# Performance work log

Measured on AMD Instinct MI355X. Metric: run time of the kernel, lower is better.

The kernel has to match this reference:

```python
import jax, jax.numpy as jnp
import numpy as np
from jax import lax

DUNITS = 1024
ATT_DIM = 512
EPROJS = 512
ACONV_CHANS = 10
ACONV_FILTS = 100  # kernel size = 2*100+1 = 201
H_LEN = 16384
N_PREV = 128
SCALING = 2.0


def setup_inputs() -> dict:
    key = jax.random.key(0)
    ks = jax.random.split(key, 10)
    inv = lambda fan_in: 1.0 / np.sqrt(fan_in)
    return {
        "dec_z": jax.random.normal(ks[0], (1, DUNITS), jnp.float32),
        "att_prev": jax.random.uniform(ks[1], (N_PREV, 1, H_LEN), jnp.float32) / H_LEN,
        "pre_compute_enc_h": jax.random.normal(ks[2], (1, H_LEN, ATT_DIM), jnp.float32),
        "enc_h": jax.random.normal(ks[3], (1, H_LEN, EPROJS), jnp.float32),
        "mask": jnp.zeros((1, H_LEN), jnp.float32),
        # parameters (torch default inits, scale by 1/sqrt(fan_in))
        "loc_conv_w": jax.random.normal(ks[4], (ACONV_CHANS, 1, 2 * ACONV_FILTS + 1), jnp.float32) * inv(2 * ACONV_FILTS + 1),
        "mlp_att_w": jax.random.normal(ks[5], (ATT_DIM, ACONV_CHANS), jnp.float32) * inv(ACONV_CHANS),
        "mlp_dec_w": jax.random.normal(ks[6], (ATT_DIM, DUNITS), jnp.float32) * inv(DUNITS),
        "gvec_w": jax.random.normal(ks[7], (1, ATT_DIM), jnp.float32) * inv(ATT_DIM),
        "gvec_b": jnp.zeros((1,), jnp.float32),
    }


def reference(dec_z, att_prev, pre_compute_enc_h, enc_h, mask,
              loc_conv_w, mlp_att_w, mlp_dec_w, gvec_w, gvec_b):
    h_length = enc_h.shape[1]
    dec_z = dec_z.reshape(1, DUNITS)

    # coverage vector: sum of all previous attention distributions -> [1, h]
    cov_vec = jnp.sum(att_prev, axis=0)

    # location conv: Conv2d(1, C, (1, 2F+1)) on [1,1,1,h] == 1D conv on [1,1,h]
    att_conv = lax.conv_general_dilated(
        cov_vec[:, None, :], loc_conv_w,
        window_strides=(1,), padding=[(ACONV_FILTS, ACONV_FILTS)],
        dimension_numbers=("NCH", "OIH", "NCH"),
    )  # [1, C, h]
    # squeeze/transpose then mlp_att (no bias): [1, h, att_dim]
    att_conv = jnp.einsum("bch,ac->bha", att_conv, mlp_att_w)

    # mlp_dec (no bias), tiled over h: [1, 1, att_dim]
    dec_z_tiled = (dec_z @ mlp_dec_w.T)[:, None, :]

    # additive attention score e: [1, h]
    t = jnp.tanh(att_conv + pre_compute_enc_h + dec_z_tiled)
    e = jnp.einsum("bha,oa->bho", t, gvec_w)[..., 0] + gvec_b
    e = e + mask

    w = jax.nn.softmax(SCALING * e, axis=1)  # [1, h]

    att_prev_new = jnp.concatenate([att_prev, w[None]], axis=0)  # [n+1, 1, h]
    c = jnp.sum(enc_h * w[:, :, None], axis=1)  # [1, eprojs]
    return (c, att_prev_new)
```

## Files before the change

### kernel.cpp

```cpp
#include <hip/hip_runtime.h>

#define H_LEN 16384
#define ATT_DIM 512
#define DUNITS 1024
#define EPROJS 512
#define NCH 10
#define KFILT 201
#define PAD 100
#define N_PREV 128
#define NB_SCORE 512
#define NB_CTX 256

__global__ __launch_bounds__(256) void k_prep(const float* __restrict__ att_prev,
                                              const float* __restrict__ mlp_dec_w,
                                              const float* __restrict__ dec_z,
                                              float* __restrict__ out_prev,
                                              float* __restrict__ cov4,
                                              float* __restrict__ dz,
                                              float* __restrict__ out_c) {
    int b = blockIdx.x, tid = threadIdx.x;
    if (b < 256) {
        int h = (b >> 2) * 256 + tid;
        int n0 = (b & 3) * 32;
        float s = 0.f;
        #pragma unroll
        for (int n = n0; n < n0 + 32; ++n) {
            float v = att_prev[n * H_LEN + h];
            s += v;
            out_prev[n * H_LEN + h] = v;
        }
        cov4[(b & 3) * H_LEN + h] = s;
    } else if (b < 384) {
        int lane = tid & 63;
        int a = (b - 256) * 4 + (tid >> 6);
        const float* row = mlp_dec_w + a * DUNITS;
        float s = 0.f;
        #pragma unroll
        for (int t = 0; t < DUNITS / 64; ++t) s += row[lane + 64 * t] * dec_z[lane + 64 * t];
        #pragma unroll
        for (int off = 32; off > 0; off >>= 1) s += __shfl_xor(s, off, 64);
        if (lane == 0) dz[a] = s;
    } else {
        out_c[tid] = 0.f;
        out_c[tid + 256] = 0.f;
    }
}

__global__ __launch_bounds__(256, 2) void k_score(const float* __restrict__ cov4,
                                                  const float* __restrict__ cw,
                                                  const float* __restrict__ pre,
                                                  const float* __restrict__ mask,
                                                  const float* __restrict__ dz,
                                                  const float* __restrict__ watt,
                                                  const float* __restrict__ gv,
                                                  const float* __restrict__ gb,
                                                  float* __restrict__ vbuf,
                                                  float* __restrict__ pm,
                                                  float* __restrict__ ps) {
    __shared__ float cov_s[32 + 2 * PAD];
    __shared__ float mask_s[32];
    __shared__ float pc[4][NCH][32];
    __shared__ float cf[NCH][32];
    __shared__ float vt[32];

    int tid = threadIdx.x, b = blockIdx.x;
    int h0 = b * 32;
    int lane = tid & 63, wv = tid >> 6;
    int a0 = lane * 4;

    for (int i = tid; i < 32 + 2 * PAD; i += 256) {
        int g = h0 - PAD + i;
        float s = 0.f;
        if (g >= 0 && g < H_LEN)
            s = cov4[g] + cov4[H_LEN + g] + cov4[2 * H_LEN + g] + cov4[3 * H_LEN + g];
        cov_s[i] = s;
    }
    if (tid < 32) mask_s[tid] = mask[h0 + tid];

    const float4* pre4 = (const float4*)pre;
    int hbase = h0 + wv * 8;
    float4 P[16];
    #pragma unroll
    for (int j = 0; j < 8; ++j) {
        P[2 * j]     = pre4[(hbase + j) * 128 + lane];
        P[2 * j + 1] = pre4[(hbase + j) * 128 + 64 + lane];
    }

    float Wr[8][NCH], dzr[8], gvr[8];
    #pragma unroll
    for (int i = 0; i < 8; ++i) {
        int a = (i < 4) ? (a0 + i) : (a0 + 256 + (i - 4));
        dzr[i] = dz[a];
        gvr[i] = gv[a];
        #pragma unroll
        for (int c = 0; c < NCH; ++c) Wr[i][c] = watt[a * NCH + c];
    }
    float bias = gb[0];
    __syncthreads();

    {
        int h = tid & 31, q = tid >> 5;
        int k0 = (q * KFILT) / 8, k1 = ((q + 1) * KFILT) / 8;
        float acc[NCH];
        #pragma unroll
        for (int c = 0; c < NCH; ++c) acc[c] = 0.f;
        for (int k = k0; k < k1; ++k) {
            float s = cov_s[h + k];
            #pragma unroll
            for (int c = 0; c < NCH; ++c) acc[c] += s * cw[c * KFILT + k];
        }
        #pragma unroll
        for (int c = 0; c < NCH; ++c) pc[q & 3][c][h] = acc[c];
        __syncthreads();
        if (q >= 4) {
            #pragma unroll
            for (int c = 0; c < NCH; ++c) atomicAdd(&pc[q & 3][c][h], 0.f);
        }
    }
    __syncthreads();
    for (int i = tid; i < NCH * 32; i += 256) {
        int c = i >> 5, h = i & 31;
        cf[c][h] = pc[0][c][h] + pc[1][c][h] + pc[2][c][h] + pc[3][c][h];
    }
    __syncthreads();

    #pragma unroll
    for (int j = 0; j < 8; ++j) {
        int hh = wv * 8 + j;
        float ch[NCH];
        #pragma unroll
        for (int c = 0; c < NCH; ++c) ch[c] = cf[c][hh];
        float4 c0 = P[2 * j], c1 = P[2 * j + 1];
        float pv[8] = {c0.x, c0.y, c0.z, c0.w, c1.x, c1.y, c1.z, c1.w};
        float eacc = 0.f;
        #pragma unroll
        for (int i = 0; i < 8; ++i) {
            float x = pv[i] + dzr[i];
            #pragma unroll
            for (int c = 0; c < NCH; ++c) x += ch[c] * Wr[i][c];
            x = fminf(fmaxf(x, -15.f), 15.f);
            float z = __expf(2.f * x);
            float t = (z - 1.f) * __builtin_amdgcn_rcpf(z + 1.f);
            eacc += t * gvr[i];
        }
        #pragma unroll
        for (int off = 32; off > 0; off >>= 1) eacc += __shfl_xor(eacc, off, 64);
        if (lane == 0) {
            float v = 2.f * (eacc + bias + mask_s[hh]);
            vt[hh] = v;
            vbuf[h0 + hh] = v;
        }
    }
    __syncthreads();

    if (wv == 0) {
        float v = (lane < 32) ? vt[lane] : -1e30f;
        float m = v;
        #pragma unroll
        for (int off = 32; off > 0; off >>= 1) m = fmaxf(m, __shfl_xor(m, off, 64));
        float s = (lane < 32) ? __expf(v - m) : 0.f;
        #pragma unroll
        for (int off = 32; off > 0; off >>= 1) s += __shfl_xor(s, off, 64);
        if (lane == 0) { pm[b] = m; ps[b] = s; }
    }
}

__global__ __launch_bounds__(512) void k_ctx(const float* __restrict__ vbuf,
                                             const float* __restrict__ pm,
                                             const float* __restrict__ ps,
                                             const float* __restrict__ enc,
                                             float* __restrict__ out_w,
                                             float* __restrict__ out_c) {
    __shared__ float redA[8], redB[8];
    __shared__ float wlds[64];
    int tid = threadIdx.x, b = blockIdx.x;
    int lane = tid & 63, wv = tid >> 6;
    int h0 = b * 64;

    float pmv = pm[tid], psv = ps[tid];
    float m = pmv;
    #pragma unroll
    for (int off = 32; off > 0; off >>= 1) m = fmaxf(m, __shfl_xor(m, off, 64));
    if (lane == 0) redA[wv] = m;
    __syncthreads();
    float M = redA[0];
    #pragma unroll
    for (int i = 1; i < 8; ++i) M = fmaxf(M, redA[i]);
    float s = psv * __expf(pmv - M);
    #pragma unroll
    for (int off = 32; off > 0; off >>= 1) s += __shfl_xor(s, off, 64);
    if (lane == 0) redB[wv] = s;
    __syncthreads();
    float S = 0.f;
    #pragma unroll
    for (int i = 0; i < 8; ++i) S += redB[i];
    float rinv = 1.f / S;

    if (tid < 64) {
        float w = __expf(vbuf[h0 + tid] - M) * rinv;
        out_w[h0 + tid] = w;
        wlds[tid] = w;
    }
    __syncthreads();
    float acc = 0.f;
    #pragma unroll 8
    for (int i = 0; i < 64; ++i) acc += wlds[i] * enc[(h0 + i) * EPROJS + tid];
    atomicAdd(&out_c[tid], acc);
}

extern "C" void kernel_launch(void* const* d_in, const int* in_sizes, int n_in,
                              void* d_out, int out_size, void* d_ws, size_t ws_size,
                              hipStream_t stream) {
    const float* dec_z      = (const float*)d_in[0];
    const float* att_prev   = (const float*)d_in[1];
    const float* pre        = (const float*)d_in[2];
    const float* enc_h      = (const float*)d_in[3];
    const float* mask       = (const float*)d_in[4];
    const float* loc_conv_w = (const float*)d_in[5];
    const float* mlp_att_w  = (const float*)d_in[6];
    const float* mlp_dec_w  = (const float*)d_in[7];
    const float* gvec_w     = (const float*)d_in[8];
    const float* gvec_b     = (const float*)d_in[9];

    float* out_c    = (float*)d_out;
    float* out_prev = out_c + EPROJS;
    float* out_w    = out_prev + N_PREV * H_LEN;

    float* ws   = (float*)d_ws;
    float* cov4 = ws;
    float* dz   = cov4 + 4 * H_LEN;
    float* vb   = dz + ATT_DIM;
    float* pm   = vb + H_LEN;
    float* ps   = pm + NB_SCORE;

    k_prep<<<385, 256, 0, stream>>>(att_prev, mlp_dec_w, dec_z, out_prev, cov4, dz, out_c);
    k_score<<<NB_SCORE, 256, 0, stream>>>(cov4, loc_conv_w, pre, mask, dz, mlp_att_w,
                                          gvec_w, gvec_b, vb, pm, ps);
    k_ctx<<<NB_CTX, 512, 0, stream>>>(vb, pm, ps, enc_h, out_w, out_c);
}
```

Baseline: 145.9 us.

## Fuse context accumulation into score kernel using flash-style partial softmax rescaling

Each score block now multiplies its local unnormalized exp weights against its 32 rows of enc_h and writes a per-block partial context vector. A small final kernel computes the global max and sum, rescales each block's partial, and atomically accumulates into the output. This moves the enc_h read into the score kernel, where it can overlap with the tanh work, and shrinks the last kernel to a reduction. The conv partial-sum step also drops the LDS atomic trick in favour of an 8-way buffer. The cost is an extra 1 MB workspace for the partials and more register pressure in k_score.

```diff
diff --git a/kernel.cpp b/kernel.cpp
--- a/kernel.cpp
+++ b/kernel.cpp
@@ -9,7 +9,7 @@
 #define PAD 100
 #define N_PREV 128
 #define NB_SCORE 512
-#define NB_CTX 256
+#define NB_FIN 256
 
 __global__ __launch_bounds__(256) void k_prep(const float* __restrict__ att_prev,
                                               const float* __restrict__ mlp_dec_w,
@@ -54,14 +54,17 @@
                                                   const float* __restrict__ watt,
                                                   const float* __restrict__ gv,
                                                   const float* __restrict__ gb,
+                                                  const float* __restrict__ enc,
                                                   float* __restrict__ vbuf,
                                                   float* __restrict__ pm,
-                                                  float* __restrict__ ps) {
+                                                  float* __restrict__ ps,
+                                                  float* __restrict__ pcb) {
     __shared__ float cov_s[32 + 2 * PAD];
     __shared__ float mask_s[32];
-    __shared__ float pc[4][NCH][32];
+    __shared__ float pc[8][NCH][32];
     __shared__ float cf[NCH][32];
     __shared__ float vt[32];
+    __shared__ float wt[32];
 
     int tid = threadIdx.x, b = blockIdx.x;
     int h0 = b * 32;
@@ -110,17 +113,15 @@
             for (int c = 0; c < NCH; ++c) acc[c] += s * cw[c * KFILT + k];
         }
         #pragma unroll
-        for (int c = 0; c < NCH; ++c) pc[q & 3][c][h] = acc[c];
-        __syncthreads();
-        if (q >= 4) {
-            #pragma unroll
-            for (int c = 0; c < NCH; ++c) atomicAdd(&pc[q & 3][c][h], 0.f);
-        }
+        for (int c = 0; c < NCH; ++c) pc[q][c][h] = acc[c];
     }
     __syncthreads();
     for (int i = tid; i < NCH * 32; i += 256) {
         int c = i >> 5, h = i & 31;
-        cf[c][h] = pc[0][c][h] + pc[1][c][h] + pc[2][c][h] + pc[3][c][h];
+        float s = 0.f;
+        #pragma unroll
+        for (int q = 0; q < 8; ++q) s += pc[q][c][h];
+        cf[c][h] = s;
     }
     __syncthreads();
 
@@ -158,54 +159,65 @@
         float m = v;
         #pragma unroll
         for (int off = 32; off > 0; off >>= 1) m = fmaxf(m, __shfl_xor(m, off, 64));
-        float s = (lane < 32) ? __expf(v - m) : 0.f;
+        float ev = (lane < 32) ? __expf(v - m) : 0.f;
+        if (lane < 32) wt[lane] = ev;
+        float s = ev;
         #pragma unroll
         for (int off = 32; off > 0; off >>= 1) s += __shfl_xor(s, off, 64);
         if (lane == 0) { pm[b] = m; ps[b] = s; }
     }
-}
-
-__global__ __launch_bounds__(512) void k_ctx(const float* __restrict__ vbuf,
-                                             const float* __restrict__ pm,
-                                             const float* __restrict__ ps,
-                                             const float* __restrict__ enc,
-                                             float* __restrict__ out_w,
-                                             float* __restrict__ out_c) {
-    __shared__ float redA[8], redB[8];
-    __shared__ float wlds[64];
+    __syncthreads();
+
+    const float2* enc2 = (const float2*)enc;
+    float2 acc = {0.f, 0.f};
+    #pragma unroll 4
+    for (int h = 0; h < 32; ++h) {
+        float wl = wt[h];
+        float2 ev = enc2[(h0 + h) * 256 + tid];
+        acc.x += wl * ev.x;
+        acc.y += wl * ev.y;
+    }
+    ((float2*)pcb)[b * 256 + tid] = acc;
+}
+
+__global__ __launch_bounds__(256) void k_final(const float* __restrict__ vbuf,
+                                               const float* __restrict__ pm,
+                                               const float* __restrict__ ps,
+                                               const float* __restrict__ pcb,
+                                               float* __restrict__ out_w,
+                                               float* __restrict__ out_c) {
+    __shared__ float redA[4], redB[4];
     int tid = threadIdx.x, b = blockIdx.x;
     int lane = tid & 63, wv = tid >> 6;
-    int h0 = b * 64;
-
-    float pmv = pm[tid], psv = ps[tid];
-    float m = pmv;
+
+    float m0 = pm[tid], m1 = pm[tid + 256];
+    float s0 = ps[tid], s1 = ps[tid + 256];
+    float m = fmaxf(m0, m1);
     #pragma unroll
     for (int off = 32; off > 0; off >>= 1) m = fmaxf(m, __shfl_xor(m, off, 64));
     if (lane == 0) redA[wv] = m;
     __syncthreads();
-    float M = redA[0];
-    #pragma unroll
-    for (int i = 1; i < 8; ++i) M = fmaxf(M, redA[i]);
-    float s = psv * __expf(pmv - M);
+    float M = fmaxf(fmaxf(redA[0], redA[1]), fmaxf(redA[2], redA[3]));
+    float s = s0 * __expf(m0 - M) + s1 * __expf(m1 - M);
     #pragma unroll
     for (int off = 32; off > 0; off >>= 1) s += __shfl_xor(s, off, 64);
     if (lane == 0) redB[wv] = s;
     __syncthreads();
-    float S = 0.f;
-    #pragma unroll
-    for (int i = 0; i < 8; ++i) S += redB[i];
+    float S = redB[0] + redB[1] + redB[2] + redB[3];
     float rinv = 1.f / S;
 
     if (tid < 64) {
-        float w = __expf(vbuf[h0 + tid] - M) * rinv;
-        out_w[h0 + tid] = w;
-        wlds[tid] = w;
-    }
-    __syncthreads();
-    float acc = 0.f;
-    #pragma unroll 8
-    for (int i = 0; i < 64; ++i) acc += wlds[i] * enc[(h0 + i) * EPROJS + tid];
-    atomicAdd(&out_c[tid], acc);
+        int h = b * 64 + tid;
+        out_w[h] = __expf(vbuf[h] - M) * rinv;
+    }
+
+    int r0 = 2 * b, r1 = 2 * b + 1;
+    float sc0 = __expf(pm[r0] - M) * rinv;
+    float sc1 = __expf(pm[r1] - M) * rinv;
+    float v0 = pcb[r0 * EPROJS + tid] * sc0 + pcb[r1 * EPROJS + tid] * sc1;
+    float v1 = pcb[r0 * EPROJS + tid + 256] * sc0 + pcb[r1 * EPROJS + tid + 256] * sc1;
+    atomicAdd(&out_c[tid], v0);
+    atomicAdd(&out_c[tid + 256], v1);
 }
 
 extern "C" void kernel_launch(void* const* d_in, const int* in_sizes, int n_in,
@@ -232,9 +244,10 @@
     float* vb   = dz + ATT_DIM;
     float* pm   = vb + H_LEN;
     float* ps   = pm + NB_SCORE;
+    float* pcb  = ps + NB_SCORE;
 
     k_prep<<<385, 256, 0, stream>>>(att_prev, mlp_dec_w, dec_z, out_prev, cov4, dz, out_c);
     k_score<<<NB_SCORE, 256, 0, stream>>>(cov4, loc_conv_w, pre, mask, dz, mlp_att_w,
-                                          gvec_w, gvec_b, vb, pm, ps);
-    k_ctx<<<NB_CTX, 512, 0, stream>>>(vb, pm, ps, enc_h, out_w, out_c);
-}
+                                          gvec_w, gvec_b, enc_h, vb, pm, ps, pcb);
+    k_final<<<NB_FIN, 256, 0, stream>>>(vb, pm, ps, pcb, out_w, out_c);
+}
```

After: 144.9 us. Within noise of the previous version (-0.7%).
